# Optimization experiments

Measured on AMD Instinct MI355X. Metric: run time of the kernel, lower is better.

Reference implementation:

```python
import jax, jax.numpy as jnp
import numpy as np
jax.config.update("jax_enable_x64", True)

B = 262144  # number of independent 8x8 DLT systems
COORD_SCALE = 128.0  # pixel-like coordinate magnitude


def setup_inputs() -> dict:
    key = jax.random.key(0)
    k1, k2 = jax.random.split(key)
    x = jax.random.normal(k1, (B, 8), dtype=jnp.float32) * COORD_SCALE
    x_p = jax.random.normal(k2, (B, 8), dtype=jnp.float32) * COORD_SCALE
    return {"x": x, "x_p": x_p}


def _dlt(x, x_p):
    Bsz = x.shape[0]
    # [B,4,2] points; u/v are [B,4]
    pts = x.reshape(-1, 4, 2).astype(jnp.float64)
    pts_p = x_p.reshape(-1, 4, 2).astype(jnp.float64)
    u, v = pts[..., 0], pts[..., 1]
    up, vp = pts_p[..., 0], pts_p[..., 1]
    zeros = jnp.zeros_like(u)
    ones = jnp.ones_like(u)
    # Faithful to torch source: the stacked A rows are cast with .long(),
    # which truncates toward zero and detaches gradients.
    rows_x = jnp.stack([zeros, zeros, zeros, -u, -v, -ones, vp * u, vp * v], axis=2)  # [B,4,8]
    rows_y = jnp.stack([u, v, ones, zeros, zeros, zeros, -up * u, -up * v], axis=2)   # [B,4,8]
    rows_x = jax.lax.stop_gradient(jnp.trunc(rows_x))
    rows_y = jax.lax.stop_gradient(jnp.trunc(rows_y))
    # Interleave so rows [0,2,4,6] = rows_x, rows [1,3,5,7] = rows_y
    A = jnp.stack([rows_x, rows_y], axis=2).reshape(Bsz, 8, 8)
    b = jnp.stack([-vp, up], axis=2).reshape(Bsz, 8, 1)
    h = jnp.linalg.pinv(A) @ b  # [B,8,1]
    H = jnp.concatenate([h, jnp.ones((Bsz, 1, 1), dtype=jnp.float64)], axis=1)
    return H.reshape(Bsz, 3, 3)


def reference(x, x_p):
    return _dlt(x, x_p)
```

## Files before the change

### kernel.cpp

```cpp
#include <hip/hip_runtime.h>
#include <hip/hip_bf16.h>
#include <math.h>

__global__ __launch_bounds__(256) void TensorDlt_48215302865189_kernel(
    const float* __restrict__ x, const float* __restrict__ xp,
    float* __restrict__ out, int B) {
  int i = blockIdx.x * blockDim.x + threadIdx.x;
  if (i >= B) return;

  const float4* x4 = reinterpret_cast<const float4*>(x + (size_t)i * 8);
  float4 a0 = x4[0], a1 = x4[1];
  const float4* p4 = reinterpret_cast<const float4*>(xp + (size_t)i * 8);
  float4 c0 = p4[0], c1 = p4[1];

  double u[4]  = {a0.x, a0.z, a1.x, a1.z};
  double v[4]  = {a0.y, a0.w, a1.y, a1.w};
  double up[4] = {c0.x, c0.z, c1.x, c1.z};
  double vp[4] = {c0.y, c0.w, c1.y, c1.w};

  double A[8][9];
#pragma unroll
  for (int k = 0; k < 4; k++) {
    double U = trunc(u[k]), V = trunc(v[k]);
    double W = trunc(vp[k] * u[k]), X = trunc(vp[k] * v[k]);
    double Y = trunc(up[k] * u[k]), Z = trunc(up[k] * v[k]);
    A[2 * k][0] = 0.0;  A[2 * k][1] = 0.0;  A[2 * k][2] = 0.0;
    A[2 * k][3] = -U;   A[2 * k][4] = -V;   A[2 * k][5] = -1.0;
    A[2 * k][6] = W;    A[2 * k][7] = X;    A[2 * k][8] = -vp[k];
    A[2 * k + 1][0] = U;   A[2 * k + 1][1] = V;   A[2 * k + 1][2] = 1.0;
    A[2 * k + 1][3] = 0.0; A[2 * k + 1][4] = 0.0; A[2 * k + 1][5] = 0.0;
    A[2 * k + 1][6] = -Y;  A[2 * k + 1][7] = -Z;  A[2 * k + 1][8] = up[k];
  }

#pragma unroll
  for (int k = 0; k < 8; k++) {
#pragma unroll
    for (int r = k + 1; r < 8; r++) {
      bool sw = fabs(A[r][k]) > fabs(A[k][k]);
#pragma unroll
      for (int c = k; c < 9; c++) {
        double t0 = A[k][c], t1 = A[r][c];
        A[k][c] = sw ? t1 : t0;
        A[r][c] = sw ? t0 : t1;
      }
    }
    double pinv = 1.0 / A[k][k];
#pragma unroll
    for (int r = k + 1; r < 8; r++) {
      double f = A[r][k] * pinv;
#pragma unroll
      for (int c = k + 1; c < 9; c++) A[r][c] -= f * A[k][c];
    }
  }

  double h[8];
#pragma unroll
  for (int k = 7; k >= 0; k--) {
    double s = A[k][8];
#pragma unroll
    for (int c = k + 1; c < 8; c++) s -= A[k][c] * h[c];
    h[k] = s / A[k][k];
  }

  float* o = out + (size_t)i * 9;
#pragma unroll
  for (int k = 0; k < 8; k++) o[k] = (float)h[k];
  o[8] = 1.0f;
}

extern "C" void kernel_launch(void* const* d_in, const int* in_sizes, int n_in,
                              void* d_out, int out_size, void* d_ws, size_t ws_size,
                              hipStream_t stream) {
  const float* x  = (const float*)d_in[0];
  const float* xp = (const float*)d_in[1];
  float* out = (float*)d_out;
  int B = in_sizes[0] / 8;
  int block = 256;
  int grid = (B + block - 1) / block;
  TensorDlt_48215302865189_kernel<<<grid, block, 0, stream>>>(x, xp, out, B);
}
```

Baseline: 72.04 us.

## Replace generic 8x8 Gaussian elimination with closed-form block-structured DLT solve

Replaces the fully unrolled partial-pivoting 8x8 elimination with a closed-form solve that uses the DLT matrix structure. Three points are eliminated through a 3x3 adjugate, leaving a 2x2 system for h6 and h7, with the point triple picked by largest determinant magnitude. This removes most of the fp64 arithmetic and register pressure of the generic solver. In exchange, numerical behaviour can differ from pivoted elimination on ill-conditioned inputs.

Result: faster. 67.07 us (-6.9%).

```diff
diff --git a/kernel.cpp b/kernel.cpp
--- a/kernel.cpp
+++ b/kernel.cpp
@@ -18,54 +18,81 @@
   double up[4] = {c0.x, c0.z, c1.x, c1.z};
   double vp[4] = {c0.y, c0.w, c1.y, c1.w};
 
-  double A[8][9];
+  double U[4], V[4], Y[4], Z[4], W[4], X[4];
 #pragma unroll
   for (int k = 0; k < 4; k++) {
-    double U = trunc(u[k]), V = trunc(v[k]);
-    double W = trunc(vp[k] * u[k]), X = trunc(vp[k] * v[k]);
-    double Y = trunc(up[k] * u[k]), Z = trunc(up[k] * v[k]);
-    A[2 * k][0] = 0.0;  A[2 * k][1] = 0.0;  A[2 * k][2] = 0.0;
-    A[2 * k][3] = -U;   A[2 * k][4] = -V;   A[2 * k][5] = -1.0;
-    A[2 * k][6] = W;    A[2 * k][7] = X;    A[2 * k][8] = -vp[k];
-    A[2 * k + 1][0] = U;   A[2 * k + 1][1] = V;   A[2 * k + 1][2] = 1.0;
-    A[2 * k + 1][3] = 0.0; A[2 * k + 1][4] = 0.0; A[2 * k + 1][5] = 0.0;
-    A[2 * k + 1][6] = -Y;  A[2 * k + 1][7] = -Z;  A[2 * k + 1][8] = up[k];
+    U[k] = trunc(u[k]);
+    V[k] = trunc(v[k]);
+    Y[k] = trunc(up[k] * u[k]);
+    Z[k] = trunc(up[k] * v[k]);
+    W[k] = trunc(vp[k] * u[k]);
+    X[k] = trunc(vp[k] * v[k]);
   }
 
-#pragma unroll
-  for (int k = 0; k < 8; k++) {
-#pragma unroll
-    for (int r = k + 1; r < 8; r++) {
-      bool sw = fabs(A[r][k]) > fabs(A[k][k]);
-#pragma unroll
-      for (int c = k; c < 9; c++) {
-        double t0 = A[k][c], t1 = A[r][c];
-        A[k][c] = sw ? t1 : t0;
-        A[r][c] = sw ? t0 : t1;
-      }
-    }
-    double pinv = 1.0 / A[k][k];
-#pragma unroll
-    for (int r = k + 1; r < 8; r++) {
-      double f = A[r][k] * pinv;
-#pragma unroll
-      for (int c = k + 1; c < 9; c++) A[r][c] -= f * A[k][c];
-    }
+  double d3 = U[0] * (V[1] - V[2]) + U[1] * (V[2] - V[0]) + U[2] * (V[0] - V[1]);
+  double d2 = U[0] * (V[1] - V[3]) + U[1] * (V[3] - V[0]) + U[3] * (V[0] - V[1]);
+  double d1 = U[0] * (V[2] - V[3]) + U[2] * (V[3] - V[0]) + U[3] * (V[0] - V[2]);
+  double d0 = U[1] * (V[2] - V[3]) + U[2] * (V[3] - V[1]) + U[3] * (V[1] - V[2]);
+
+  int e = 3;
+  double bd = fabs(d3);
+  if (fabs(d2) > bd) { e = 2; bd = fabs(d2); }
+  if (fabs(d1) > bd) { e = 1; bd = fabs(d1); }
+  if (fabs(d0) > bd) { e = 0; bd = fabs(d0); }
+
+#define PERM4(a)                                                             \
+  {                                                                          \
+    double p0 = (e == 0) ? a[1] : a[0];                                      \
+    double p1 = (e >= 2) ? a[1] : a[2];                                      \
+    double p2 = (e == 3) ? a[2] : a[3];                                      \
+    double p3 = (e == 3) ? a[3] : (e == 2) ? a[2] : (e == 1) ? a[1] : a[0];  \
+    a[0] = p0; a[1] = p1; a[2] = p2; a[3] = p3;                              \
   }
+  PERM4(U); PERM4(V); PERM4(Y); PERM4(Z); PERM4(W); PERM4(X);
+  PERM4(up); PERM4(vp);
+#undef PERM4
 
-  double h[8];
-#pragma unroll
-  for (int k = 7; k >= 0; k--) {
-    double s = A[k][8];
-#pragma unroll
-    for (int c = k + 1; c < 8; c++) s -= A[k][c] * h[c];
-    h[k] = s / A[k][k];
-  }
+  double N00 = V[1] - V[2], N01 = V[2] - V[0], N02 = V[0] - V[1];
+  double N10 = U[2] - U[1], N11 = U[0] - U[2], N12 = U[1] - U[0];
+  double N20 = U[1] * V[2] - V[1] * U[2];
+  double N21 = U[2] * V[0] - V[2] * U[0];
+  double N22 = U[0] * V[1] - V[0] * U[1];
+  double det = U[0] * N00 + V[0] * N10 + N20;
+
+  double q0 = U[3] * N00 + V[3] * N10 + N20;
+  double q1 = U[3] * N01 + V[3] * N11 + N21;
+  double q2 = U[3] * N02 + V[3] * N12 + N22;
+
+  double A1 = q0 * Y[0] + q1 * Y[1] + q2 * Y[2] - det * Y[3];
+  double B1 = q0 * Z[0] + q1 * Z[1] + q2 * Z[2] - det * Z[3];
+  double R1 = det * up[3] - (q0 * up[0] + q1 * up[1] + q2 * up[2]);
+  double A2 = q0 * W[0] + q1 * W[1] + q2 * W[2] - det * W[3];
+  double B2 = q0 * X[0] + q1 * X[1] + q2 * X[2] - det * X[3];
+  double R2 = det * vp[3] - (q0 * vp[0] + q1 * vp[1] + q2 * vp[2]);
+
+  double D2inv = 1.0 / (A1 * B2 - A2 * B1);
+  double h6 = (R1 * B2 - R2 * B1) * D2inv;
+  double h7 = (A1 * R2 - A2 * R1) * D2inv;
+
+  double detinv = 1.0 / det;
+  double r0 = up[0] + Y[0] * h6 + Z[0] * h7;
+  double r1 = up[1] + Y[1] * h6 + Z[1] * h7;
+  double r2 = up[2] + Y[2] * h6 + Z[2] * h7;
+  double h0 = (N00 * r0 + N01 * r1 + N02 * r2) * detinv;
+  double h1 = (N10 * r0 + N11 * r1 + N12 * r2) * detinv;
+  double h2 = (N20 * r0 + N21 * r1 + N22 * r2) * detinv;
+
+  double s0 = vp[0] + W[0] * h6 + X[0] * h7;
+  double s1 = vp[1] + W[1] * h6 + X[1] * h7;
+  double s2 = vp[2] + W[2] * h6 + X[2] * h7;
+  double h3 = (N00 * s0 + N01 * s1 + N02 * s2) * detinv;
+  double h4 = (N10 * s0 + N11 * s1 + N12 * s2) * detinv;
+  double h5 = (N20 * s0 + N21 * s1 + N22 * s2) * detinv;
 
   float* o = out + (size_t)i * 9;
-#pragma unroll
-  for (int k = 0; k < 8; k++) o[k] = (float)h[k];
-  o[8] = 1.0f;
+  o[0] = (float)h0; o[1] = (float)h1; o[2] = (float)h2;
+  o[3] = (float)h3; o[4] = (float)h4; o[5] = (float)h5;
+  o[6] = (float)h6; o[7] = (float)h7; o[8] = 1.0f;
 }
 
 extern "C" void kernel_launch(void* const* d_in, const int* in_sizes, int n_in,
```
